# Kernel optimization log

Hardware: AMD Instinct MI355X
Metric: run time of the kernel (lower is better)

The kernel has to match this reference:

```python
import jax, jax.numpy as jnp
import numpy as np
import math

B, S, D, H = 4, 2048, 1024, 16
DK = D // H  # 64
THETA = 10000.0


def setup_inputs() -> dict:
    key = jax.random.key(0)
    ks = jax.random.split(key, 5)
    std = 0.02
    return {
        "x": jax.random.normal(ks[0], (B, S, D), dtype=jnp.float32),
        "Wq": jax.random.normal(ks[1], (D, D), dtype=jnp.float32) * std,
        "Wk": jax.random.normal(ks[2], (D, D), dtype=jnp.float32) * std,
        "Wv": jax.random.normal(ks[3], (D, D), dtype=jnp.float32) * std,
        "Wo": jax.random.normal(ks[4], (D, D), dtype=jnp.float32) * std / math.sqrt(2 * 12),
        "token_positions": jnp.arange(S, dtype=jnp.int32),
    }


def _rope(x, pos):
    # x: [B, H, S, DK]; pos: [S]. Interleaved-pair rotary embedding.
    inv_freq = THETA ** (-jnp.arange(0, DK, 2, dtype=jnp.float32) / DK)  # [DK/2]
    ang = pos.astype(jnp.float32)[:, None] * inv_freq[None, :]  # [S, DK/2]
    cos, sin = jnp.cos(ang), jnp.sin(ang)
    x1, x2 = x[..., 0::2], x[..., 1::2]  # [B, H, S, DK/2]
    r1 = x1 * cos - x2 * sin
    r2 = x1 * sin + x2 * cos
    return jnp.stack([r1, r2], axis=-1).reshape(x.shape)


def reference(x, Wq, Wk, Wv, Wo, token_positions):
    b, s, d = x.shape
    Q = x @ Wq
    K = x @ Wk
    V = x @ Wv
    # [B, S, D] -> [B, H, S, DK]
    def split(t):
        return t.reshape(b, s, H, DK).transpose(0, 2, 1, 3)
    Qh, Kh, Vh = split(Q), split(K), split(V)
    Qh = _rope(Qh, token_positions)
    Kh = _rope(Kh, token_positions)
    scores = jnp.einsum('bhqd,bhkd->bhqk', Qh, Kh) / math.sqrt(DK)
    causal = jnp.tril(jnp.ones((s, s), dtype=bool))
    scores = jnp.where(causal, scores, -jnp.inf)
    probs = jax.nn.softmax(scores, axis=-1)
    out = jnp.einsum('bhqk,bhkd->bhqd', probs, Vh)
    out = out.transpose(0, 2, 1, 3).reshape(b, s, d)
    return out @ Wo
```

## Files before the change

kernel.cpp:

```cpp
#include <hip/hip_runtime.h>
#include <hip/hip_bf16.h>

#define B_N 4
#define S_LEN 2048
#define D_MODEL 1024
#define N_HEAD 16
#define D_HEAD 64
#define M_ROWS (B_N * S_LEN)

typedef short bf16x8 __attribute__((ext_vector_type(8)));
typedef short bf16x4 __attribute__((ext_vector_type(4)));
typedef float f32x4 __attribute__((ext_vector_type(4)));

#if __has_builtin(__builtin_amdgcn_mfma_f32_16x16x16bf16_1k)
#define HAVE_MFMA16 1
#else
#define HAVE_MFMA16 0
#endif

__device__ __forceinline__ unsigned short f2bf(float f) {
  union { float f; unsigned int u; } v; v.f = f;
  unsigned int r = v.u + 0x7FFFu + ((v.u >> 16) & 1u);
  return (unsigned short)(r >> 16);
}
__device__ __forceinline__ float bf2f(unsigned short u) {
  union { unsigned int u; float f; } v; v.u = ((unsigned int)u) << 16;
  return v.f;
}
__device__ __forceinline__ unsigned int pkbf(float a, float b) {
  union { __hip_bfloat162 h; unsigned int u; } cv;
  cv.h = __float22bfloat162_rn(make_float2(a, b));
  return cv.u;
}
__device__ __forceinline__ bf16x8 ld8(const unsigned short* p) {
  return *reinterpret_cast<const bf16x8*>(p);
}
__device__ __forceinline__ bf16x4 ld4(const unsigned short* p) {
  return *reinterpret_cast<const bf16x4*>(p);
}
__device__ __forceinline__ void glds16(const unsigned short* g, unsigned short* l) {
  __builtin_amdgcn_global_load_lds(
      (const __attribute__((address_space(1))) unsigned int*)g,
      (__attribute__((address_space(3))) unsigned int*)l, 16, 0, 0);
}

__global__ __launch_bounds__(256) void rope_tab_k(const int* __restrict__ pos,
                                                  float2* __restrict__ tab) {
  const int idx = blockIdx.x * 256 + threadIdx.x;
  const int s = idx >> 5;
  const int i = idx & 31;
  const float inv = exp2f(-(float)i * 0.41524101186092029f);
  const float ang = (float)pos[s] * inv;
  tab[idx] = make_float2(cosf(ang), sinf(ang));
}

__global__ __launch_bounds__(256) void cast_k(const float* __restrict__ X,
                                              unsigned short* __restrict__ Y) {
  const size_t i = ((size_t)blockIdx.x * 256 + threadIdx.x) * 8;
  const float4 a = *reinterpret_cast<const float4*>(X + i);
  const float4 b = *reinterpret_cast<const float4*>(X + i + 4);
  union { unsigned int u[4]; uint4 v; } o;
  o.u[0] = pkbf(a.x, a.y); o.u[1] = pkbf(a.z, a.w);
  o.u[2] = pkbf(b.x, b.y); o.u[3] = pkbf(b.z, b.w);
  *reinterpret_cast<uint4*>(Y + i) = o.v;
}

__global__ __launch_bounds__(256) void wtrans_k(
    const float* __restrict__ W0, const float* __restrict__ W1,
    const float* __restrict__ W2, const float* __restrict__ W3,
    unsigned short* __restrict__ T0, unsigned short* __restrict__ T1,
    unsigned short* __restrict__ T2, unsigned short* __restrict__ T3) {
  const int z = blockIdx.z;
  const float* __restrict__ W = (z == 0) ? W0 : (z == 1) ? W1 : (z == 2) ? W2 : W3;
  unsigned short* __restrict__ T = (z == 0) ? T0 : (z == 1) ? T1 : (z == 2) ? T2 : T3;
  __shared__ __align__(16) unsigned short tile[64][72];
  const int kb = blockIdx.x * 64;
  const int nb = blockIdx.y * 64;
#pragma unroll
  for (int it = 0; it < 2; ++it) {
    const int chunk = it * 256 + threadIdx.x;
    const int r = chunk >> 3;
    const int c8 = (chunk & 7) * 8;
    const float* src = W + (size_t)(kb + r) * D_MODEL + nb + c8;
    const float4 a = *reinterpret_cast<const float4*>(src);
    const float4 b = *reinterpret_cast<const float4*>(src + 4);
    union { unsigned int u[4]; uint4 v; } o;
    o.u[0] = pkbf(a.x, a.y); o.u[1] = pkbf(a.z, a.w);
    o.u[2] = pkbf(b.x, b.y); o.u[3] = pkbf(b.z, b.w);
    *reinterpret_cast<uint4*>(&tile[r][c8]) = o.v;
  }
  __syncthreads();
#pragma unroll
  for (int it = 0; it < 2; ++it) {
    const int chunk = it * 256 + threadIdx.x;
    const int n = chunk >> 3;
    const int k8 = (chunk & 7) * 8;
    __align__(16) unsigned short vals[8];
#pragma unroll
    for (int j = 0; j < 8; ++j) vals[j] = tile[k8 + j][n];
    *reinterpret_cast<uint4*>(T + (size_t)(nb + n) * D_MODEL + kb + k8) =
        *reinterpret_cast<const uint4*>(vals);
  }
}

__global__ __launch_bounds__(256) void gemm2_k(
    const unsigned short* __restrict__ A, const unsigned short* __restrict__ W,
    float* __restrict__ OF) {
  __shared__ __align__(16) unsigned short smem[4][64][68];
  unsigned short* As = &smem[0][0][0];
  unsigned short* Bs = As + 128 * 32;

  const int tid = threadIdx.x;
  const int lane = tid & 63;
  const int w = tid >> 6;
  const int l15 = lane & 15;
  const int l4 = lane >> 4;

  const int row0 = blockIdx.x * 128;
  const int col0 = blockIdx.y * 128;

  const int srow = w * 32 + (lane >> 2);
  const int scol = (lane & 3) * 8;
  const unsigned short* ga = A + (size_t)(row0 + srow) * D_MODEL + scol;
  const unsigned short* gb = W + (size_t)(col0 + srow) * D_MODEL + scol;
  unsigned short* la = &As[(w * 32) * 32];
  unsigned short* lb = &Bs[(w * 32) * 32];

  const int wrow = (w & 1) * 64;
  const int wcol = (w >> 1) * 64;

  f32x4 acc[4][4];
  const f32x4 fz = {0.f, 0.f, 0.f, 0.f};
#pragma unroll
  for (int m = 0; m < 4; ++m)
#pragma unroll
    for (int n = 0; n < 4; ++n) acc[m][n] = fz;

  for (int kb = 0; kb < D_MODEL; kb += 32) {
    glds16(ga + kb, la);
    glds16(ga + 16 * D_MODEL + kb, la + 16 * 32);
    glds16(gb + kb, lb);
    glds16(gb + 16 * D_MODEL + kb, lb + 16 * 32);
    __syncthreads();
    bf16x8 af[4], bfr[4];
#pragma unroll
    for (int m = 0; m < 4; ++m) af[m] = ld8(&As[(wrow + m * 16 + l15) * 32 + l4 * 8]);
#pragma unroll
    for (int n = 0; n < 4; ++n) bfr[n] = ld8(&Bs[(wcol + n * 16 + l15) * 32 + l4 * 8]);
#pragma unroll
    for (int m = 0; m < 4; ++m)
#pragma unroll
      for (int n = 0; n < 4; ++n)
        acc[m][n] = __builtin_amdgcn_mfma_f32_16x16x32_bf16(af[m], bfr[n], acc[m][n], 0, 0, 0);
    __syncthreads();
  }

#pragma unroll
  for (int n = 0; n < 4; ++n) {
    const int gcol = col0 + wcol + n * 16 + l15;
#pragma unroll
    for (int m = 0; m < 4; ++m)
#pragma unroll
      for (int r = 0; r < 4; ++r)
        OF[(size_t)(row0 + wrow + m * 16 + l4 * 4 + r) * D_MODEL + gcol] = acc[m][n][r];
  }
}

__global__ __launch_bounds__(512, 1) void gemm8_k(
    const unsigned short* __restrict__ A, const unsigned short* __restrict__ W,
    unsigned short* __restrict__ Qo, unsigned short* __restrict__ Ko,
    unsigned short* __restrict__ VTo, const float2* __restrict__ tab) {
  __shared__ __align__(16) unsigned short smem[3][384 * 64];

  const int tid = threadIdx.x;
  const int lane = tid & 63;
  const int w = tid >> 6;
  const int l15 = lane & 15;
  const int l4 = lane >> 4;
  const int wm = w >> 2;
  const int wn = w & 3;

  const int row0 = blockIdx.x * 128;
  const int col0 = blockIdx.y * 256;

  const int srow = lane >> 3;
  const int schunk = (lane & 7) ^ srow;
  const unsigned short* gA = A + (size_t)(row0 + w * 8 + srow) * D_MODEL + schunk * 8;
  const unsigned short* gB = W + (size_t)(col0 + w * 8 + srow) * D_MODEL + schunk * 8;

  const int swz = l15 & 7;
  const int kc0 = ((l4) ^ swz) * 8;
  const int kc1 = ((l4 + 4) ^ swz) * 8;

  f32x4 acc[4][4];
  const f32x4 fz = {0.f, 0.f, 0.f, 0.f};
#pragma unroll
  for (int m = 0; m < 4; ++m)
#pragma unroll
    for (int n = 0; n < 4; ++n) acc[m][n] = fz;

#define G8_STAGE_A(SL, T)                                                      \
  do {                                                                         \
    unsigned short* sa_ = &smem[SL][(w * 8) * 64];                             \
    const unsigned short* g_ = gA + (size_t)(T) * 64;                          \
    glds16(g_, sa_);                                                           \
    glds16(g_ + 64 * D_MODEL, sa_ + 64 * 64);                                  \
  } while (0)

#define G8_STAGE_B(SL, T)                                                      \
  do {                                                                         \
    unsigned short* sb_ = &smem[SL][(128 + w * 8) * 64];                       \
    const unsigned short* g_ = gB + (size_t)(T) * 64;                          \
    glds16(g_, sb_);                                                           \
    glds16(g_ + 64 * D_MODEL, sb_ + 64 * 64);                                  \
    glds16(g_ + 128 * D_MODEL, sb_ + 128 * 64);                                \
    glds16(g_ + 192 * D_MODEL, sb_ + 192 * 64);                                \
  } while (0)

#define G8_PHASE(SL, KC, STG)                                                  \
  do {                                                                         \
    const unsigned short* As_ = &smem[SL][0];                                  \
    const unsigned short* Bs_ = &smem[SL][128 * 64];                           \
    bf16x8 af_[4], bf_[4];                                                     \
    _Pragma("unroll") for (int mi = 0; mi < 4; ++mi)                           \
      af_[mi] = ld8(As_ + (wm * 64 + mi * 16 + l15) * 64 + (KC));              \
    _Pragma("unroll") for (int ni = 0; ni < 4; ++ni)                           \
      bf_[ni] = ld8(Bs_ + (wn * 64 + ni * 16 + l15) * 64 + (KC));              \
    STG;                                                                       \
    __builtin_amdgcn_s_barrier();                                              \
    __builtin_amdgcn_s_setprio(1);                                             \
    _Pragma("unroll") for (int mi = 0; mi < 4; ++mi)                           \
      _Pragma("unroll") for (int ni = 0; ni < 4; ++ni)                         \
        acc[mi][ni] = __builtin_amdgcn_mfma_f32_16x16x32_bf16(                 \
            af_[mi], bf_[ni], acc[mi][ni], 0, 0, 0);                           \
    __builtin_amdgcn_s_setprio(0);                                             \
    __builtin_amdgcn_s_barrier();                                              \
  } while (0)

  G8_STAGE_A(0, 0); G8_STAGE_B(0, 0);
  G8_STAGE_A(1, 1); G8_STAGE_B(1, 1);

#pragma unroll
  for (int t = 0; t < 16; ++t) {
    const int sl = t % 3;
    const int sp = (t + 2) % 3;
    if (t < 15) {
      asm volatile("s_waitcnt vmcnt(6)" ::: "memory");
    } else {
      asm volatile("s_waitcnt vmcnt(0)" ::: "memory");
    }
    __builtin_amdgcn_s_barrier();
    if (t < 14) {
      G8_PHASE(sl, kc0, G8_STAGE_A(sp, (t + 2)));
      G8_PHASE(sl, kc1, G8_STAGE_B(sp, (t + 2)));
    } else {
      G8_PHASE(sl, kc0, ((void)0));
      G8_PHASE(sl, kc1, ((void)0));
    }
  }
#undef G8_STAGE_A
#undef G8_STAGE_B
#undef G8_PHASE

  unsigned short(*T)[68] =
      (unsigned short(*)[68])(&smem[0][0] + w * 4352);
  const int gcb = col0 + wn * 64;
  const bool isV = (gcb >= 2048);
  const int lr = lane >> 3;
  const int lc = lane & 7;

  if (!isV) {
#pragma unroll
    for (int mi = 0; mi < 4; ++mi)
#pragma unroll
      for (int n = 0; n < 4; ++n)
#pragma unroll
        for (int r = 0; r < 4; ++r)
          T[mi * 16 + l4 * 4 + r][n * 16 + l15] = f2bf(acc[mi][n][r]);
  } else {
#pragma unroll
    for (int mi = 0; mi < 4; ++mi)
#pragma unroll
      for (int n = 0; n < 4; ++n)
#pragma unroll
        for (int r = 0; r < 4; ++r)
          T[n * 16 + l15][mi * 16 + l4 * 4 + r] = f2bf(acc[mi][n][r]);
  }
  if (!isV) {
    const bool isQ = (gcb < 1024);
    unsigned short* O = isQ ? Qo : Ko;
    const float qs = isQ ? 0.18033688011112042f : 1.0f;
    const int cbase = gcb & 1023;
#pragma unroll
    for (int rg = 0; rg < 8; ++rg) {
      const int trow = rg * 8 + lr;
      const int grow = row0 + wm * 64 + trow;
      const int s = grow & (S_LEN - 1);
      const bf16x8 vv = ld8(&T[trow][lc * 8]);
      const float4 tA = *reinterpret_cast<const float4*>(&tab[s * 32 + lc * 4]);
      const float4 tB = *reinterpret_cast<const float4*>(&tab[s * 32 + lc * 4 + 2]);
      float x[8];
#pragma unroll
      for (int j = 0; j < 8; ++j) x[j] = bf2f((unsigned short)vv[j]);
      union { unsigned int u[4]; uint4 v; } o;
      o.u[0] = pkbf((x[0] * tA.x - x[1] * tA.y) * qs, (x[0] * tA.y + x[1] * tA.x) * qs);
      o.u[1] = pkbf((x[2] * tA.z - x[3] * tA.w) * qs, (x[2] * tA.w + x[3] * tA.z) * qs);
      o.u[2] = pkbf((x[4] * tB.x - x[5] * tB.y) * qs, (x[4] * tB.y + x[5] * tB.x) * qs);
      o.u[3] = pkbf((x[6] * tB.z - x[7] * tB.w) * qs, (x[6] * tB.w + x[7] * tB.z) * qs);
      *reinterpret_cast<uint4*>(O + (size_t)grow * D_MODEL + cbase + lc * 8) = o.v;
    }
  } else {
    const int vc0 = gcb - 2048;
    const int h = vc0 >> 6;
    const int bb = row0 >> 11;
    const int s0 = (row0 & (S_LEN - 1)) + wm * 64;
#pragma unroll
    for (int rg = 0; rg < 8; ++rg) {
      const int dk = rg * 8 + lr;
      const bf16x8 vv = ld8(&T[dk][lc * 8]);
      *reinterpret_cast<bf16x8*>(
          VTo + ((size_t)((bb << 4) + h) * 64 + dk) * S_LEN + s0 + lc * 8) = vv;
    }
  }
}

__global__ __launch_bounds__(512) void attn6_k(
    const unsigned short* __restrict__ Q, const unsigned short* __restrict__ K,
    const unsigned short* __restrict__ VT, unsigned short* __restrict__ O) {
  const int pair = blockIdx.x;
  const int h = blockIdx.y;
  const int b = blockIdx.z;
  const int tid = threadIdx.x;
  const int w = tid >> 6;
  const int lane = tid & 63;
  const int l15 = lane & 15;
  const int l4 = lane >> 4;

  __shared__ __align__(16) unsigned short Ks[64][72];
  __shared__ __align__(16) unsigned short Vs[64][72];
#if !HAVE_MFMA16
  __shared__ __align__(16) unsigned short Ps[8][16][72];
#endif

  const f32x4 fz = {0.f, 0.f, 0.f, 0.f};
  const unsigned short* kbase = K + (size_t)b * S_LEN * D_MODEL + h * D_HEAD;
  const unsigned short* vbase = VT + (size_t)((b << 4) + h) * 64 * S_LEN;

  const int rr = tid >> 3;
  const int c8 = (tid & 7) * 8;

  for (int half = 0; half < 2; ++half) {
    const int qt = half ? (15 - pair) : pair;
    const int qb = qt * 128;
    const int qw0 = qb + w * 16;

    bf16x8 qf[2];
#pragma unroll
    for (int kc = 0; kc < 2; ++kc)
      qf[kc] = ld8(Q + (size_t)(b * S_LEN + qw0 + l15) * D_MODEL +
                   h * D_HEAD + kc * 32 + l4 * 8);

    f32x4 o[4];
#pragma unroll
    for (int d = 0; d < 4; ++d) o[d] = fz;
    float lsum = 0.f;

    const int nkt = qb / 64 + 2;
    uint4 kreg = *reinterpret_cast<const uint4*>(kbase + (size_t)rr * D_MODEL + c8);
    uint4 vreg = *reinterpret_cast<const uint4*>(vbase + (size_t)rr * S_LEN + c8);

    for (int kt = 0; kt < nkt; ++kt) {
      const int kb0 = kt * 64;
      *reinterpret_cast<uint4*>(&Ks[rr][c8]) = kreg;
      *reinterpret_cast<uint4*>(&Vs[rr][c8]) = vreg;
      if (kt + 1 < nkt) {
        const int nb0 = kb0 + 64;
        kreg = *reinterpret_cast<const uint4*>(kbase + (size_t)(nb0 + rr) * D_MODEL + c8);
        vreg = *reinterpret_cast<const uint4*>(vbase + (size_t)rr * S_LEN + nb0 + c8);
      }
      __syncthreads();

      if (kb0 <= qw0 + 15) {
        f32x4 s[4];
#pragma unroll
        for (int n = 0; n < 4; ++n) {
          const bf16x8 kf0 = ld8(&Ks[n * 16 + l15][l4 * 8]);
          const bf16x8 kf1 = ld8(&Ks[n * 16 + l15][32 + l4 * 8]);
          f32x4 a0 = __builtin_amdgcn_mfma_f32_16x16x32_bf16(kf0, qf[0], fz, 0, 0, 0);
          s[n] = __builtin_amdgcn_mfma_f32_16x16x32_bf16(kf1, qf[1], a0, 0, 0, 0);
        }
        bf16x4 pf[4];
        const bool full = (kb0 + 63 <= qw0);
        const int q = qw0 + l15;
        float su = lsum;
#pragma unroll
        for (int n = 0; n < 4; ++n) {
          float e[4];
          if (full) {
#pragma unroll
            for (int r = 0; r < 4; ++r) e[r] = exp2f(s[n][r]);
          } else {
#pragma unroll
            for (int r = 0; r < 4; ++r) {
              const int key = kb0 + n * 16 + l4 * 4 + r;
              const float v = exp2f(s[n][r]);
              e[r] = (key <= q) ? v : 0.f;
            }
          }
          su += (e[0] + e[1]) + (e[2] + e[3]);
          union { unsigned int u[2]; bf16x4 v; } pk;
          pk.u[0] = pkbf(e[0], e[1]);
          pk.u[1] = pkbf(e[2], e[3]);
          pf[n] = pk.v;
        }
        lsum = su;

#if HAVE_MFMA16
#pragma unroll
        for (int d = 0; d < 4; ++d) {
          bf16x4 vfc[4];
#pragma unroll
          for (int c = 0; c < 4; ++c) vfc[c] = ld4(&Vs[d * 16 + l15][c * 16 + l4 * 4]);
#pragma unroll
          for (int c = 0; c < 4; ++c)
            o[d] = __builtin_amdgcn_mfma_f32_16x16x16bf16_1k(vfc[c], pf[c], o[d], 0, 0, 0);
        }
#else
#pragma unroll
        for (int n = 0; n < 4; ++n)
          *reinterpret_cast<bf16x4*>(&Ps[w][l15][n * 16 + l4 * 4]) = pf[n];
        bf16x8 pfr[2];
#pragma unroll
        for (int kc = 0; kc < 2; ++kc)
          pfr[kc] = ld8(&Ps[w][l15][kc * 32 + l4 * 8]);
#pragma unroll
        for (int d = 0; d < 4; ++d) {
          const bf16x8 vf0 = ld8(&Vs[d * 16 + l15][l4 * 8]);
          const bf16x8 vf1 = ld8(&Vs[d * 16 + l15][32 + l4 * 8]);
          o[d] = __builtin_amdgcn_mfma_f32_16x16x32_bf16(vf0, pfr[0], o[d], 0, 0, 0);
          o[d] = __builtin_amdgcn_mfma_f32_16x16x32_bf16(vf1, pfr[1], o[d], 0, 0, 0);
        }
#endif
      }
      __syncthreads();
    }

    float s = lsum;
    s += __shfl_xor(s, 16);
    s += __shfl_xor(s, 32);
    const float li = 1.0f / s;
    unsigned short* op = O + (size_t)(b * S_LEN + qw0 + l15) * D_MODEL +
                         h * D_HEAD + l4 * 4;
#pragma unroll
    for (int d = 0; d < 4; ++d) {
      union { unsigned int u[2]; uint2 v; } ov;
      ov.u[0] = pkbf(o[d][0] * li, o[d][1] * li);
      ov.u[1] = pkbf(o[d][2] * li, o[d][3] * li);
      *reinterpret_cast<uint2*>(op + d * 16) = ov.v;
    }
  }
}

extern "C" void kernel_launch(void* const* d_in, const int* in_sizes, int n_in,
                              void* d_out, int out_size, void* d_ws, size_t ws_size,
                              hipStream_t stream) {
  const float* x  = (const float*)d_in[0];
  const float* Wq = (const float*)d_in[1];
  const float* Wk = (const float*)d_in[2];
  const float* Wv = (const float*)d_in[3];
  const float* Wo = (const float*)d_in[4];
  const int* pos  = (const int*)d_in[5];
  float* out = (float*)d_out;

  char* ws = (char*)d_ws;
  const size_t big = (size_t)M_ROWS * D_MODEL * 2;
  const size_t wsz = (size_t)D_MODEL * D_MODEL * 2;
  unsigned short* xb  = (unsigned short*)(ws + 0 * big);
  unsigned short* Qb  = (unsigned short*)(ws + 1 * big);
  unsigned short* Kb  = (unsigned short*)(ws + 2 * big);
  unsigned short* VT  = (unsigned short*)(ws + 3 * big);
  unsigned short* Wqkvt = (unsigned short*)(ws + 4 * big);
  unsigned short* Wot   = (unsigned short*)(ws + 4 * big + 3 * wsz);
  float2* tab = (float2*)d_out;

  rope_tab_k<<<dim3(S_LEN * 32 / 256), 256, 0, stream>>>(pos, tab);
  cast_k<<<dim3(M_ROWS * D_MODEL / 2048), 256, 0, stream>>>(x, xb);
  wtrans_k<<<dim3(16, 16, 4), 256, 0, stream>>>(
      Wq, Wk, Wv, Wo, Wqkvt, Wqkvt + (size_t)D_MODEL * D_MODEL,
      Wqkvt + 2 * (size_t)D_MODEL * D_MODEL, Wot);
  gemm8_k<<<dim3(M_ROWS / 128, 3 * D_MODEL / 256), 512, 0, stream>>>(
      xb, Wqkvt, Qb, Kb, VT, tab);
  attn6_k<<<dim3(8, N_HEAD, B_N), 512, 0, stream>>>(Qb, Kb, VT, Qb);
  gemm2_k<<<dim3(M_ROWS / 128, D_MODEL / 128), 256, 0, stream>>>(Qb, Wot, out);
}
```

Before: 270.0 us.

## Shrink attention query tile to 64 rows and double-buffer K/V in LDS

The attention kernel now runs 256-thread blocks covering 64 query rows each, with twice as many blocks paired so causal work stays balanced. K/V tiles are double-buffered in shared memory: the next tile is written to the alternate buffer after compute, so each iteration needs one barrier instead of two. The diagonal-skip check is dropped because every wave now touches only tiles up to its own diagonal. Smaller blocks raise occupancy and cut wasted masked work, but each block reloads the same K/V tiles more often in total.

```diff
diff --git a/kernel.cpp b/kernel.cpp
--- a/kernel.cpp
+++ b/kernel.cpp
@@ -324,10 +324,10 @@
   }
 }
 
-__global__ __launch_bounds__(512) void attn6_k(
+__global__ __launch_bounds__(256) void attn7_k(
     const unsigned short* __restrict__ Q, const unsigned short* __restrict__ K,
     const unsigned short* __restrict__ VT, unsigned short* __restrict__ O) {
-  const int pair = blockIdx.x;
+  const int p2 = blockIdx.x;
   const int h = blockIdx.y;
   const int b = blockIdx.z;
   const int tid = threadIdx.x;
@@ -336,23 +336,24 @@
   const int l15 = lane & 15;
   const int l4 = lane >> 4;
 
-  __shared__ __align__(16) unsigned short Ks[64][72];
-  __shared__ __align__(16) unsigned short Vs[64][72];
+  __shared__ __align__(16) unsigned short Ks[2][64][72];
+  __shared__ __align__(16) unsigned short Vs[2][64][72];
 #if !HAVE_MFMA16
-  __shared__ __align__(16) unsigned short Ps[8][16][72];
+  __shared__ __align__(16) unsigned short Ps[4][16][72];
 #endif
 
   const f32x4 fz = {0.f, 0.f, 0.f, 0.f};
   const unsigned short* kbase = K + (size_t)b * S_LEN * D_MODEL + h * D_HEAD;
   const unsigned short* vbase = VT + (size_t)((b << 4) + h) * 64 * S_LEN;
 
-  const int rr = tid >> 3;
-  const int c8 = (tid & 7) * 8;
+  const int rr = tid >> 2;
+  const int cc = (tid & 3) * 16;
 
   for (int half = 0; half < 2; ++half) {
-    const int qt = half ? (15 - pair) : pair;
-    const int qb = qt * 128;
+    const int qt = half ? (31 - p2) : p2;
+    const int qb = qt * 64;
     const int qw0 = qb + w * 16;
+    const int nkt = qt + 1;
 
     bf16x8 qf[2];
 #pragma unroll
@@ -365,90 +366,107 @@
     for (int d = 0; d < 4; ++d) o[d] = fz;
     float lsum = 0.f;
 
-    const int nkt = qb / 64 + 2;
-    uint4 kreg = *reinterpret_cast<const uint4*>(kbase + (size_t)rr * D_MODEL + c8);
-    uint4 vreg = *reinterpret_cast<const uint4*>(vbase + (size_t)rr * S_LEN + c8);
+    {
+      const uint4* kp = reinterpret_cast<const uint4*>(kbase + (size_t)rr * D_MODEL + cc);
+      const uint4* vp = reinterpret_cast<const uint4*>(vbase + (size_t)rr * S_LEN + cc);
+      const uint4 a0 = kp[0], a1 = kp[1], b0 = vp[0], b1 = vp[1];
+      *reinterpret_cast<uint4*>(&Ks[0][rr][cc]) = a0;
+      *reinterpret_cast<uint4*>(&Ks[0][rr][cc + 8]) = a1;
+      *reinterpret_cast<uint4*>(&Vs[0][rr][cc]) = b0;
+      *reinterpret_cast<uint4*>(&Vs[0][rr][cc + 8]) = b1;
+    }
+    uint4 ka, kb2, va, vb2;
+    if (nkt > 1) {
+      const uint4* kp = reinterpret_cast<const uint4*>(kbase + (size_t)(64 + rr) * D_MODEL + cc);
+      const uint4* vp = reinterpret_cast<const uint4*>(vbase + (size_t)rr * S_LEN + 64 + cc);
+      ka = kp[0]; kb2 = kp[1]; va = vp[0]; vb2 = vp[1];
+    }
+    __syncthreads();
 
     for (int kt = 0; kt < nkt; ++kt) {
+      const int p = kt & 1;
       const int kb0 = kt * 64;
-      *reinterpret_cast<uint4*>(&Ks[rr][c8]) = kreg;
-      *reinterpret_cast<uint4*>(&Vs[rr][c8]) = vreg;
+
+      f32x4 s[4];
+#pragma unroll
+      for (int n = 0; n < 4; ++n) {
+        const bf16x8 kf0 = ld8(&Ks[p][n * 16 + l15][l4 * 8]);
+        const bf16x8 kf1 = ld8(&Ks[p][n * 16 + l15][32 + l4 * 8]);
+        f32x4 a0 = __builtin_amdgcn_mfma_f32_16x16x32_bf16(kf0, qf[0], fz, 0, 0, 0);
+        s[n] = __builtin_amdgcn_mfma_f32_16x16x32_bf16(kf1, qf[1], a0, 0, 0, 0);
+      }
+      bf16x4 pf[4];
+      const bool full = (kb0 + 63 <= qw0);
+      const int q = qw0 + l15;
+      float su = lsum;
+#pragma unroll
+      for (int n = 0; n < 4; ++n) {
+        float e[4];
+        if (full) {
+#pragma unroll
+          for (int r = 0; r < 4; ++r) e[r] = exp2f(s[n][r]);
+        } else {
+#pragma unroll
+          for (int r = 0; r < 4; ++r) {
+            const int key = kb0 + n * 16 + l4 * 4 + r;
+            const float v = exp2f(s[n][r]);
+            e[r] = (key <= q) ? v : 0.f;
+          }
+        }
+        su += (e[0] + e[1]) + (e[2] + e[3]);
+        union { unsigned int u[2]; bf16x4 v; } pk;
+        pk.u[0] = pkbf(e[0], e[1]);
+        pk.u[1] = pkbf(e[2], e[3]);
+        pf[n] = pk.v;
+      }
+      lsum = su;
+
+#if HAVE_MFMA16
+#pragma unroll
+      for (int d = 0; d < 4; ++d) {
+        bf16x4 vfc[4];
+#pragma unroll
+        for (int c = 0; c < 4; ++c) vfc[c] = ld4(&Vs[p][d * 16 + l15][c * 16 + l4 * 4]);
+#pragma unroll
+        for (int c = 0; c < 4; ++c)
+          o[d] = __builtin_amdgcn_mfma_f32_16x16x16bf16_1k(vfc[c], pf[c], o[d], 0, 0, 0);
+      }
+#else
+#pragma unroll
+      for (int n = 0; n < 4; ++n)
+        *reinterpret_cast<bf16x4*>(&Ps[w][l15][n * 16 + l4 * 4]) = pf[n];
+      bf16x8 pfr[2];
+#pragma unroll
+      for (int kc = 0; kc < 2; ++kc)
+        pfr[kc] = ld8(&Ps[w][l15][kc * 32 + l4 * 8]);
+#pragma unroll
+      for (int d = 0; d < 4; ++d) {
+        const bf16x8 vf0 = ld8(&Vs[p][d * 16 + l15][l4 * 8]);
+        const bf16x8 vf1 = ld8(&Vs[p][d * 16 + l15][32 + l4 * 8]);
+        o[d] = __builtin_amdgcn_mfma_f32_16x16x32_bf16(vf0, pfr[0], o[d], 0, 0, 0);
+        o[d] = __builtin_amdgcn_mfma_f32_16x16x32_bf16(vf1, pfr[1], o[d], 0, 0, 0);
+      }
+#endif
+
       if (kt + 1 < nkt) {
-        const int nb0 = kb0 + 64;
-        kreg = *reinterpret_cast<const uint4*>(kbase + (size_t)(nb0 + rr) * D_MODEL + c8);
-        vreg = *reinterpret_cast<const uint4*>(vbase + (size_t)rr * S_LEN + nb0 + c8);
+        *reinterpret_cast<uint4*>(&Ks[1 - p][rr][cc]) = ka;
+        *reinterpret_cast<uint4*>(&Ks[1 - p][rr][cc + 8]) = kb2;
+        *reinterpret_cast<uint4*>(&Vs[1 - p][rr][cc]) = va;
+        *reinterpret_cast<uint4*>(&Vs[1 - p][rr][cc + 8]) = vb2;
+        if (kt + 2 < nkt) {
+          const int nb0 = kb0 + 128;
+          const uint4* kp = reinterpret_cast<const uint4*>(kbase + (size_t)(nb0 + rr) * D_MODEL + cc);
+          const uint4* vp = reinterpret_cast<const uint4*>(vbase + (size_t)rr * S_LEN + nb0 + cc);
+          ka = kp[0]; kb2 = kp[1]; va = vp[0]; vb2 = vp[1];
+        }
       }
       __syncthreads();
-
-      if (kb0 <= qw0 + 15) {
-        f32x4 s[4];
-#pragma unroll
-        for (int n = 0; n < 4; ++n) {
-          const bf16x8 kf0 = ld8(&Ks[n * 16 + l15][l4 * 8]);
-          const bf16x8 kf1 = ld8(&Ks[n * 16 + l15][32 + l4 * 8]);
-          f32x4 a0 = __builtin_amdgcn_mfma_f32_16x16x32_bf16(kf0, qf[0], fz, 0, 0, 0);
-          s[n] = __builtin_amdgcn_mfma_f32_16x16x32_bf16(kf1, qf[1], a0, 0, 0, 0);
-        }
-        bf16x4 pf[4];
-        const bool full = (kb0 + 63 <= qw0);
-        const int q = qw0 + l15;
-        float su = lsum;
-#pragma unroll
-        for (int n = 0; n < 4; ++n) {
-          float e[4];
-          if (full) {
-#pragma unroll
-            for (int r = 0; r < 4; ++r) e[r] = exp2f(s[n][r]);
-          } else {
-#pragma unroll
-            for (int r = 0; r < 4; ++r) {
-              const int key = kb0 + n * 16 + l4 * 4 + r;
-              const float v = exp2f(s[n][r]);
-              e[r] = (key <= q) ? v : 0.f;
-            }
-          }
-          su += (e[0] + e[1]) + (e[2] + e[3]);
-          union { unsigned int u[2]; bf16x4 v; } pk;
-          pk.u[0] = pkbf(e[0], e[1]);
-          pk.u[1] = pkbf(e[2], e[3]);
-          pf[n] = pk.v;
-        }
-        lsum = su;
-
-#if HAVE_MFMA16
-#pragma unroll
-        for (int d = 0; d < 4; ++d) {
-          bf16x4 vfc[4];
-#pragma unroll
-          for (int c = 0; c < 4; ++c) vfc[c] = ld4(&Vs[d * 16 + l15][c * 16 + l4 * 4]);
-#pragma unroll
-          for (int c = 0; c < 4; ++c)
-            o[d] = __builtin_amdgcn_mfma_f32_16x16x16bf16_1k(vfc[c], pf[c], o[d], 0, 0, 0);
-        }
-#else
-#pragma unroll
-        for (int n = 0; n < 4; ++n)
-          *reinterpret_cast<bf16x4*>(&Ps[w][l15][n * 16 + l4 * 4]) = pf[n];
-        bf16x8 pfr[2];
-#pragma unroll
-        for (int kc = 0; kc < 2; ++kc)
-          pfr[kc] = ld8(&Ps[w][l15][kc * 32 + l4 * 8]);
-#pragma unroll
-        for (int d = 0; d < 4; ++d) {
-          const bf16x8 vf0 = ld8(&Vs[d * 16 + l15][l4 * 8]);
-          const bf16x8 vf1 = ld8(&Vs[d * 16 + l15][32 + l4 * 8]);
-          o[d] = __builtin_amdgcn_mfma_f32_16x16x32_bf16(vf0, pfr[0], o[d], 0, 0, 0);
-          o[d] = __builtin_amdgcn_mfma_f32_16x16x32_bf16(vf1, pfr[1], o[d], 0, 0, 0);
-        }
-#endif
-      }
-      __syncthreads();
-    }
-
-    float s = lsum;
-    s += __shfl_xor(s, 16);
-    s += __shfl_xor(s, 32);
-    const float li = 1.0f / s;
+    }
+
+    float s2 = lsum;
+    s2 += __shfl_xor(s2, 16);
+    s2 += __shfl_xor(s2, 32);
+    const float li = 1.0f / s2;
     unsigned short* op = O + (size_t)(b * S_LEN + qw0 + l15) * D_MODEL +
                          h * D_HEAD + l4 * 4;
 #pragma unroll
@@ -490,6 +508,6 @@
       Wqkvt + 2 * (size_t)D_MODEL * D_MODEL, Wot);
   gemm8_k<<<dim3(M_ROWS / 128, 3 * D_MODEL / 256), 512, 0, stream>>>(
       xb, Wqkvt, Qb, Kb, VT, tab);
-  attn6_k<<<dim3(8, N_HEAD, B_N), 512, 0, stream>>>(Qb, Kb, VT, Qb);
+  attn7_k<<<dim3(16, N_HEAD, B_N), 256, 0, stream>>>(Qb, Kb, VT, Qb);
   gemm2_k<<<dim3(M_ROWS / 128, D_MODEL / 128), 256, 0, stream>>>(Qb, Wot, out);
 }
```

After: 281.6 us. 4.3% more time.

## Process two 16-row query groups per warp in attention, doubling query tile

Applied to the files above, without the earlier changes.

Each warp now handles 32 query rows (two 16-row groups) instead of 16, so each block covers 256 queries and the grid halves to 4x16x4 blocks. Each K/V tile loaded into shared memory and each K/V fragment read from LDS is reused across twice as many queries, which cuts global and LDS traffic per unit of work. The cost is higher register pressure (launch bounds set to one block per SM). With only 256 blocks there is less parallelism, and causal load balance is coarser, which risks idle compute units.

```diff
diff --git a/kernel.cpp b/kernel.cpp
--- a/kernel.cpp
+++ b/kernel.cpp
@@ -324,10 +324,10 @@
   }
 }
 
-__global__ __launch_bounds__(512) void attn6_k(
+__global__ __launch_bounds__(512, 1) void attn8_k(
     const unsigned short* __restrict__ Q, const unsigned short* __restrict__ K,
     const unsigned short* __restrict__ VT, unsigned short* __restrict__ O) {
-  const int pair = blockIdx.x;
+  const int p4 = blockIdx.x;
   const int h = blockIdx.y;
   const int b = blockIdx.z;
   const int tid = threadIdx.x;
@@ -350,22 +350,26 @@
   const int c8 = (tid & 7) * 8;
 
   for (int half = 0; half < 2; ++half) {
-    const int qt = half ? (15 - pair) : pair;
-    const int qb = qt * 128;
-    const int qw0 = qb + w * 16;
-
-    bf16x8 qf[2];
-#pragma unroll
-    for (int kc = 0; kc < 2; ++kc)
-      qf[kc] = ld8(Q + (size_t)(b * S_LEN + qw0 + l15) * D_MODEL +
-                   h * D_HEAD + kc * 32 + l4 * 8);
-
-    f32x4 o[4];
-#pragma unroll
-    for (int d = 0; d < 4; ++d) o[d] = fz;
-    float lsum = 0.f;
-
-    const int nkt = qb / 64 + 2;
+    const int qt = half ? (7 - p4) : p4;
+    const int qb = qt * 256;
+    const int qw0 = qb + w * 32;
+
+    bf16x8 qf[2][2];
+#pragma unroll
+    for (int g = 0; g < 2; ++g)
+#pragma unroll
+      for (int kc = 0; kc < 2; ++kc)
+        qf[g][kc] = ld8(Q + (size_t)(b * S_LEN + qw0 + g * 16 + l15) * D_MODEL +
+                        h * D_HEAD + kc * 32 + l4 * 8);
+
+    f32x4 o[2][4];
+#pragma unroll
+    for (int g = 0; g < 2; ++g)
+#pragma unroll
+      for (int d = 0; d < 4; ++d) o[g][d] = fz;
+    float lsum[2] = {0.f, 0.f};
+
+    const int nkt = qb / 64 + 4;
     uint4 kreg = *reinterpret_cast<const uint4*>(kbase + (size_t)rr * D_MODEL + c8);
     uint4 vreg = *reinterpret_cast<const uint4*>(vbase + (size_t)rr * S_LEN + c8);
 
@@ -380,40 +384,46 @@
       }
       __syncthreads();
 
-      if (kb0 <= qw0 + 15) {
-        f32x4 s[4];
+      if (kb0 <= qw0 + 31) {
+        f32x4 s[2][4];
 #pragma unroll
         for (int n = 0; n < 4; ++n) {
           const bf16x8 kf0 = ld8(&Ks[n * 16 + l15][l4 * 8]);
           const bf16x8 kf1 = ld8(&Ks[n * 16 + l15][32 + l4 * 8]);
-          f32x4 a0 = __builtin_amdgcn_mfma_f32_16x16x32_bf16(kf0, qf[0], fz, 0, 0, 0);
-          s[n] = __builtin_amdgcn_mfma_f32_16x16x32_bf16(kf1, qf[1], a0, 0, 0, 0);
+#pragma unroll
+          for (int g = 0; g < 2; ++g) {
+            f32x4 a0 = __builtin_amdgcn_mfma_f32_16x16x32_bf16(kf0, qf[g][0], fz, 0, 0, 0);
+            s[g][n] = __builtin_amdgcn_mfma_f32_16x16x32_bf16(kf1, qf[g][1], a0, 0, 0, 0);
+          }
         }
-        bf16x4 pf[4];
-        const bool full = (kb0 + 63 <= qw0);
-        const int q = qw0 + l15;
-        float su = lsum;
-#pragma unroll
-        for (int n = 0; n < 4; ++n) {
-          float e[4];
-          if (full) {
-#pragma unroll
-            for (int r = 0; r < 4; ++r) e[r] = exp2f(s[n][r]);
-          } else {
-#pragma unroll
-            for (int r = 0; r < 4; ++r) {
-              const int key = kb0 + n * 16 + l4 * 4 + r;
-              const float v = exp2f(s[n][r]);
-              e[r] = (key <= q) ? v : 0.f;
+        bf16x4 pf[2][4];
+#pragma unroll
+        for (int g = 0; g < 2; ++g) {
+          const int qg = qw0 + g * 16 + l15;
+          const bool full = (kb0 + 63 <= qw0 + g * 16);
+          float su = lsum[g];
+#pragma unroll
+          for (int n = 0; n < 4; ++n) {
+            float e[4];
+            if (full) {
+#pragma unroll
+              for (int r = 0; r < 4; ++r) e[r] = exp2f(s[g][n][r]);
+            } else {
+#pragma unroll
+              for (int r = 0; r < 4; ++r) {
+                const int key = kb0 + n * 16 + l4 * 4 + r;
+                const float v = exp2f(s[g][n][r]);
+                e[r] = (key <= qg) ? v : 0.f;
+              }
             }
+            su += (e[0] + e[1]) + (e[2] + e[3]);
+            union { unsigned int u[2]; bf16x4 v; } pk;
+            pk.u[0] = pkbf(e[0], e[1]);
+            pk.u[1] = pkbf(e[2], e[3]);
+            pf[g][n] = pk.v;
           }
-          su += (e[0] + e[1]) + (e[2] + e[3]);
-          union { unsigned int u[2]; bf16x4 v; } pk;
-          pk.u[0] = pkbf(e[0], e[1]);
-          pk.u[1] = pkbf(e[2], e[3]);
-          pf[n] = pk.v;
+          lsum[g] = su;
         }
-        lsum = su;
 
 #if HAVE_MFMA16
 #pragma unroll
@@ -422,41 +432,49 @@
 #pragma unroll
           for (int c = 0; c < 4; ++c) vfc[c] = ld4(&Vs[d * 16 + l15][c * 16 + l4 * 4]);
 #pragma unroll
-          for (int c = 0; c < 4; ++c)
-            o[d] = __builtin_amdgcn_mfma_f32_16x16x16bf16_1k(vfc[c], pf[c], o[d], 0, 0, 0);
+          for (int g = 0; g < 2; ++g)
+#pragma unroll
+            for (int c = 0; c < 4; ++c)
+              o[g][d] = __builtin_amdgcn_mfma_f32_16x16x16bf16_1k(vfc[c], pf[g][c], o[g][d], 0, 0, 0);
         }
 #else
 #pragma unroll
-        for (int n = 0; n < 4; ++n)
-          *reinterpret_cast<bf16x4*>(&Ps[w][l15][n * 16 + l4 * 4]) = pf[n];
-        bf16x8 pfr[2];
-#pragma unroll
-        for (int kc = 0; kc < 2; ++kc)
-          pfr[kc] = ld8(&Ps[w][l15][kc * 32 + l4 * 8]);
-#pragma unroll
-        for (int d = 0; d < 4; ++d) {
-          const bf16x8 vf0 = ld8(&Vs[d * 16 + l15][l4 * 8]);
-          const bf16x8 vf1 = ld8(&Vs[d * 16 + l15][32 + l4 * 8]);
-          o[d] = __builtin_amdgcn_mfma_f32_16x16x32_bf16(vf0, pfr[0], o[d], 0, 0, 0);
-          o[d] = __builtin_amdgcn_mfma_f32_16x16x32_bf16(vf1, pfr[1], o[d], 0, 0, 0);
+        for (int g = 0; g < 2; ++g) {
+#pragma unroll
+          for (int n = 0; n < 4; ++n)
+            *reinterpret_cast<bf16x4*>(&Ps[w][l15][n * 16 + l4 * 4]) = pf[g][n];
+          bf16x8 pfr[2];
+#pragma unroll
+          for (int kc = 0; kc < 2; ++kc)
+            pfr[kc] = ld8(&Ps[w][l15][kc * 32 + l4 * 8]);
+#pragma unroll
+          for (int d = 0; d < 4; ++d) {
+            const bf16x8 vf0 = ld8(&Vs[d * 16 + l15][l4 * 8]);
+            const bf16x8 vf1 = ld8(&Vs[d * 16 + l15][32 + l4 * 8]);
+            o[g][d] = __builtin_amdgcn_mfma_f32_16x16x32_bf16(vf0, pfr[0], o[g][d], 0, 0, 0);
+            o[g][d] = __builtin_amdgcn_mfma_f32_16x16x32_bf16(vf1, pfr[1], o[g][d], 0, 0, 0);
+          }
         }
 #endif
       }
       __syncthreads();
     }
 
-    float s = lsum;
-    s += __shfl_xor(s, 16);
-    s += __shfl_xor(s, 32);
-    const float li = 1.0f / s;
-    unsigned short* op = O + (size_t)(b * S_LEN + qw0 + l15) * D_MODEL +
-                         h * D_HEAD + l4 * 4;
-#pragma unroll
-    for (int d = 0; d < 4; ++d) {
-      union { unsigned int u[2]; uint2 v; } ov;
-      ov.u[0] = pkbf(o[d][0] * li, o[d][1] * li);
-      ov.u[1] = pkbf(o[d][2] * li, o[d][3] * li);
-      *reinterpret_cast<uint2*>(op + d * 16) = ov.v;
+#pragma unroll
+    for (int g = 0; g < 2; ++g) {
+      float s2 = lsum[g];
+      s2 += __shfl_xor(s2, 16);
+      s2 += __shfl_xor(s2, 32);
+      const float li = 1.0f / s2;
+      unsigned short* op = O + (size_t)(b * S_LEN + qw0 + g * 16 + l15) * D_MODEL +
+                           h * D_HEAD + l4 * 4;
+#pragma unroll
+      for (int d = 0; d < 4; ++d) {
+        union { unsigned int u[2]; uint2 v; } ov;
+        ov.u[0] = pkbf(o[g][d][0] * li, o[g][d][1] * li);
+        ov.u[1] = pkbf(o[g][d][2] * li, o[g][d][3] * li);
+        *reinterpret_cast<uint2*>(op + d * 16) = ov.v;
+      }
     }
   }
 }
@@ -490,6 +508,6 @@
       Wqkvt + 2 * (size_t)D_MODEL * D_MODEL, Wot);
   gemm8_k<<<dim3(M_ROWS / 128, 3 * D_MODEL / 256), 512, 0, stream>>>(
       xb, Wqkvt, Qb, Kb, VT, tab);
-  attn6_k<<<dim3(8, N_HEAD, B_N), 512, 0, stream>>>(Qb, Kb, VT, Qb);
+  attn8_k<<<dim3(4, N_HEAD, B_N), 512, 0, stream>>>(Qb, Kb, VT, Qb);
   gemm2_k<<<dim3(M_ROWS / 128, D_MODEL / 128), 256, 0, stream>>>(Qb, Wot, out);
 }
```

New measurement: 274.6 us. No clear change (+1.7%).
